# Kernel optimization log

Hardware: AMD Instinct MI355X
Metric: run time of the kernel (lower is better)

Reference implementation:

```python
import jax, jax.numpy as jnp
import numpy as np

B, S, D = 4, 1024, 1024
H, DK, DV = 16, 64, 64


def setup_inputs() -> dict:
    key = jax.random.key(0)
    ks = jax.random.split(key, 8)
    sc = 0.02
    return {
        "queries": jax.random.normal(ks[0], (B, S, D), jnp.float32),
        "keys": jax.random.normal(ks[1], (B, S, D), jnp.float32),
        "values": jax.random.normal(ks[2], (B, S, D), jnp.float32),
        "attn_bias": jax.random.normal(ks[3], (B, 1, S, S), jnp.float32),
        "Wq": jax.random.normal(ks[4], (H * DK, D), jnp.float32) * sc,
        "Wk": jax.random.normal(ks[5], (H * DK, D), jnp.float32) * sc,
        "Wv": jax.random.normal(ks[6], (H * DV, D), jnp.float32) * sc,
        "Wp": jax.random.normal(ks[7], (D, H * DV), jnp.float32) * sc,
    }


def reference(queries, keys, values, attn_bias, Wq, Wk, Wv, Wp):
    # Linear (no bias): x @ W.T, then split heads -> [B, H, S, d]
    q = (queries @ Wq.T).reshape(B, S, H, DK).transpose(0, 2, 1, 3)
    k = (keys @ Wk.T).reshape(B, S, H, DK).transpose(0, 2, 1, 3)
    v = (values @ Wv.T).reshape(B, S, H, DV).transpose(0, 2, 1, 3)
    # NOTE: original scales by d_model**-0.5, not d_key**-0.5
    scores = jnp.einsum("bhqd,bhkd->bhqk", q, k) * (D ** -0.5)
    scores = scores + attn_bias  # bias broadcasts over heads
    weights = jax.nn.softmax(scores, axis=-1)
    out = jnp.einsum("bhqk,bhkd->bhqd", weights, v)  # [B,H,S,DV]
    out = out.transpose(0, 2, 1, 3).reshape(B, S, H * DV)
    return out @ Wp.T
```

## Files before the change

### kernel.cpp

```cpp
#include <hip/hip_runtime.h>
#include <hip/hip_bf16.h>

typedef unsigned short u16;
typedef unsigned int u32;
typedef __attribute__((ext_vector_type(8))) short bf16x8;
typedef __attribute__((ext_vector_type(8))) u16 u16x8;
typedef __attribute__((ext_vector_type(4))) u16 u16x4;
typedef __attribute__((ext_vector_type(4))) u32 u32x4;
typedef __attribute__((ext_vector_type(4))) float f32x4;
typedef __attribute__((ext_vector_type(4))) _Float16 f16x4;
typedef __attribute__((ext_vector_type(8))) _Float16 f16x8;
typedef __attribute__((ext_vector_type(16))) float f32x16;

typedef const __attribute__((address_space(1))) void* gas1_t;
typedef __attribute__((address_space(3))) void* las3_t;

#define MFMA16(a,b,c) __builtin_amdgcn_mfma_f32_16x16x32_bf16((a),(b),(c),0,0,0)
#define MFMA32(a,b,c) __builtin_amdgcn_mfma_f32_32x32x16_bf16((a),(b),(c),0,0,0)

static constexpr int BB = 4, SS = 1024, DD = 1024, HH = 16;

static __device__ __forceinline__ u16 f2b(float x) {
  union { __hip_bfloat16 h; u16 u; } cv;
  cv.h = __float2bfloat16(x);
  return cv.u;
}
static __device__ __forceinline__ u32 pk2(float a, float b) {
  return (u32)f2b(a) | ((u32)f2b(b) << 16);
}

__global__ __launch_bounds__(256) void cvt_all(
    const float* __restrict__ q, const float* __restrict__ k, const float* __restrict__ v,
    const float* __restrict__ wq_, const float* __restrict__ wk_, const float* __restrict__ wv_,
    const float* __restrict__ wp_,
    u16* __restrict__ qb, u16* __restrict__ kb, u16* __restrict__ vb,
    u16* __restrict__ wqb, u16* __restrict__ wkb, u16* __restrict__ wvb, u16* __restrict__ wpb) {
  int bid = blockIdx.x;
  const float* s; u16* d; int off;
  if      (bid < 4096)  { s = q;   d = qb;  off = bid; }
  else if (bid < 8192)  { s = k;   d = kb;  off = bid - 4096; }
  else if (bid < 12288) { s = v;   d = vb;  off = bid - 8192; }
  else if (bid < 13312) { s = wq_; d = wqb; off = bid - 12288; }
  else if (bid < 14336) { s = wk_; d = wkb; off = bid - 13312; }
  else if (bid < 15360) { s = wv_; d = wvb; off = bid - 14336; }
  else                  { s = wp_; d = wpb; off = bid - 15360; }
  int i = (off * 256 + threadIdx.x) * 4;
  float4 val = *(const float4*)(s + i);
  u16x4 r = { f2b(val.x), f2b(val.y), f2b(val.z), f2b(val.w) };
  *(u16x4*)(d + i) = r;
}

__global__ __launch_bounds__(256) void cvt_bias(const float* __restrict__ src,
                                                _Float16* __restrict__ dst) {
  int i = (blockIdx.x * 256 + threadIdx.x) * 4;
  int row = i >> 10;
  int k = i & 1023;
  int kt = k >> 6, j = k & 63;
  int hi = (j >> 2) & 1, kb = j >> 5, rq = (j >> 3) & 3;
  int idx = hi * 32 + kb * 16 + rq * 4;
  int byte_in_slice = ((((idx >> 3) ^ (row & 7)) << 4) | ((idx & 7) << 1));
  float4 v = *(const float4*)(src + i);
  f16x4 r = { (_Float16)v.x, (_Float16)v.y, (_Float16)v.z, (_Float16)v.w };
  char* p = (char*)dst + ((size_t)row * 1024 + kt * 64) * 2 + byte_in_slice;
  *(f16x4*)p = r;
}

template<typename OT, bool VTRANS>
__global__ __launch_bounds__(256) void gemm_bt(
    const u16* __restrict__ Abase, const u16* __restrict__ Wbase, OT* __restrict__ Cbase,
    u16* __restrict__ Tout, int N, int K, size_t sA, size_t sW, size_t sC) {
  const u16* A = Abase + (size_t)blockIdx.z * sA;
  const u16* W = Wbase + (size_t)blockIdx.z * sW;
  OT* C = Cbase + (size_t)blockIdx.z * sC;

  __shared__ __align__(16) u16 As[128 * 64];
  __shared__ __align__(16) u16 Bs[128 * 64];

  const int tid = threadIdx.x;
  const int lane = tid & 63;
  const int wid = tid >> 6;
  const int g = lane >> 4;
  const int li = lane & 15;

  const int hw = blockIdx.x + (blockIdx.y << 3);
  const int L = ((hw & 7) << 5) + (hw >> 3);
  const int brow = (L >> 3) * 128;
  const int bcol = (L & 7) * 128;

  const int wr = (wid >> 1) * 64;
  const int wc = (wid & 1) * 64;

  const int srow = wid * 8 + (lane >> 3);
  const int schunk = (lane & 7) ^ (lane >> 3);
  const u16* ga0 = A + (size_t)(brow + srow) * K + schunk * 8;
  const u16* gw0 = W + (size_t)(bcol + srow) * K + schunk * 8;

  f32x4 acc[4][4] = {};

  for (int k0 = 0; k0 < K; k0 += 64) {
#pragma unroll
    for (int i = 0; i < 4; ++i) {
      __builtin_amdgcn_global_load_lds((gas1_t)(const void*)(ga0 + (size_t)(i * 32) * K + k0),
                                       (las3_t)(void*)(As + (i * 32 + wid * 8) * 64), 16, 0, 0);
      __builtin_amdgcn_global_load_lds((gas1_t)(const void*)(gw0 + (size_t)(i * 32) * K + k0),
                                       (las3_t)(void*)(Bs + (i * 32 + wid * 8) * 64), 16, 0, 0);
    }
    __syncthreads();

#pragma unroll
    for (int kk = 0; kk < 2; ++kk) {
      bf16x8 a[4], b[4];
#pragma unroll
      for (int m = 0; m < 4; ++m) {
        int row = wr + m * 16 + li;
        a[m] = *(const bf16x8*)&As[row * 64 + (((kk * 4 + g) ^ (li & 7)) << 3)];
      }
#pragma unroll
      for (int n = 0; n < 4; ++n) {
        int row = wc + n * 16 + li;
        b[n] = *(const bf16x8*)&Bs[row * 64 + (((kk * 4 + g) ^ (li & 7)) << 3)];
      }
#pragma unroll
      for (int m = 0; m < 4; ++m)
#pragma unroll
        for (int n = 0; n < 4; ++n)
          acc[m][n] = MFMA16(a[m], b[n], acc[m][n]);
    }
    __syncthreads();
  }

  if (VTRANS && blockIdx.z == 2) {
#pragma unroll
    for (int m = 0; m < 4; ++m) {
#pragma unroll
      for (int n = 0; n < 4; ++n) {
        int c = bcol + wc + n * 16 + li;
        int h_ = c >> 6, dv = c & 63;
        int r0 = brow + wr + m * 16 + g * 4;
        int b_ = r0 >> 10, s0 = r0 & 1023;
        u16x4 val = { f2b(acc[m][n][0]), f2b(acc[m][n][1]),
                      f2b(acc[m][n][2]), f2b(acc[m][n][3]) };
        *(u16x4*)&Tout[(size_t)((b_ * HH + h_) * 64 + dv) * SS + s0] = val;
      }
    }
  } else {
#pragma unroll
    for (int m = 0; m < 4; ++m)
#pragma unroll
      for (int n = 0; n < 4; ++n)
#pragma unroll
        for (int j = 0; j < 4; ++j) {
          int r = brow + wr + m * 16 + g * 4 + j;
          int c = bcol + wc + n * 16 + li;
          if constexpr (sizeof(OT) == 2) C[(size_t)r * N + c] = (OT)f2b(acc[m][n][j]);
          else                           C[(size_t)r * N + c] = acc[m][n][j];
        }
  }
}

__global__ __launch_bounds__(256) void attn_kernel(
    const u16* __restrict__ Q, const u16* __restrict__ K, const u16* __restrict__ Vt,
    const _Float16* __restrict__ bias16, u16* __restrict__ O) {
  __shared__ __align__(16) u16 kbuf[2][64 * 64];
  __shared__ __align__(16) u16 vbuf[2][64 * 64];
  __shared__ __align__(16) u16 bbuf[2][8192];

  const int tid = threadIdx.x;
  const int lane = tid & 63;
  const int wq = tid >> 6;
  const int hi = lane >> 5;
  const int ln = lane & 31;
  const u32 swz = (u32)(ln & 7) << 4;

  const int flat = blockIdx.x + (blockIdx.y << 3) + (blockIdx.z << 7);
  const int L = ((flat & 7) << 6) | (flat >> 3);
  const int qt = L & 7, h = (L >> 3) & 15, b = L >> 7;
  const int q0 = qt * 128;
  const int qrow = q0 + wq * 32 + ln;

  bf16x8 qf[4];
  {
    const u16* qp = Q + (size_t)(b * SS + qrow) * DD + h * 64 + hi * 8;
#pragma unroll
    for (int d = 0; d < 4; ++d) qf[d] = *(const bf16x8*)(qp + d * 16);
  }

  const int srow = (lane >> 3);
  const int spc = ((lane & 7) ^ srow) * 8;
  const u16* kgl = K + (size_t)(b * SS + wq * 16 + srow) * DD + h * 64 + spc;
  const u16* vgl = Vt + (size_t)((b * HH + h) * 64 + wq * 16 + srow) * SS + spc;

  const _Float16* bgl = bias16 + (size_t)(b * SS + q0 + wq * 32 + srow) * SS + (lane & 7) * 8;

  const int qq = wq * 32 + ln;
  int baddr[4];
#pragma unroll
  for (int g = 0; g < 4; ++g)
    baddr[g] = qq * 128 + (((hi * 4 + g) ^ (ln & 7)) << 4);

  {
    char* bd = (char*)bbuf[0] + wq * 4096;
#pragma unroll
    for (int i = 0; i < 4; ++i)
      __builtin_amdgcn_global_load_lds((gas1_t)(const void*)(bgl + (size_t)(i * 8) * SS),
                                       (las3_t)(void*)(bd + i * 1024), 16, 0, 0);
    char* kd = (char*)kbuf[0] + wq * 2048;
    char* vd = (char*)vbuf[0] + wq * 2048;
#pragma unroll
    for (int j = 0; j < 2; ++j) {
      __builtin_amdgcn_global_load_lds((gas1_t)(const void*)(kgl + (size_t)(j * 8) * DD),
                                       (las3_t)(void*)(kd + j * 1024), 16, 0, 0);
      __builtin_amdgcn_global_load_lds((gas1_t)(const void*)(vgl + (size_t)(j * 8) * SS),
                                       (las3_t)(void*)(vd + j * 1024), 16, 0, 0);
    }
  }
  __syncthreads();

  f32x16 o0 = {}, o1 = {};
  float m = -1e30f, lsum = 0.f;
  int cur = 0;

  for (int kt = 0; kt < 16; ++kt) {
    if (kt < 15) {
      char* bd = (char*)bbuf[cur ^ 1] + wq * 4096;
      const _Float16* bs = bgl + (kt + 1) * 64;
#pragma unroll
      for (int i = 0; i < 4; ++i)
        __builtin_amdgcn_global_load_lds((gas1_t)(const void*)(bs + (size_t)(i * 8) * SS),
                                         (las3_t)(void*)(bd + i * 1024), 16, 0, 0);
      char* kd = (char*)kbuf[cur ^ 1] + wq * 2048;
      char* vd = (char*)vbuf[cur ^ 1] + wq * 2048;
      const size_t k1 = (size_t)(kt + 1) * 64;
#pragma unroll
      for (int j = 0; j < 2; ++j) {
        __builtin_amdgcn_global_load_lds((gas1_t)(const void*)(kgl + (k1 + j * 8) * DD),
                                         (las3_t)(void*)(kd + j * 1024), 16, 0, 0);
        __builtin_amdgcn_global_load_lds((gas1_t)(const void*)(vgl + (size_t)(j * 8) * SS + k1),
                                         (las3_t)(void*)(vd + j * 1024), 16, 0, 0);
      }
    }

    const char* kb_base = (const char*)kbuf[cur];
    f32x16 s[2];
#pragma unroll
    for (int kb = 0; kb < 2; ++kb) {
      f32x16 acc = {};
#pragma unroll
      for (int d = 0; d < 4; ++d) {
        bf16x8 kf = *(const bf16x8*)(kb_base + (kb * 32 + ln) * 128 + (((u32)(d * 32 + hi * 16)) ^ swz));
        acc = MFMA32(kf, qf[d], acc);
      }
      s[kb] = acc;
    }

    {
      const char* bbr = (const char*)bbuf[cur];
#pragma unroll
      for (int g = 0; g < 4; ++g) {
        f16x8 bv = *(const f16x8*)(bbr + baddr[g]);
        const int kb = g >> 1, rq0 = (g & 1) * 2;
#pragma unroll
        for (int e = 0; e < 8; ++e)
          s[kb][(rq0 + (e >> 2)) * 4 + (e & 3)] =
              fmaf(s[kb][(rq0 + (e >> 2)) * 4 + (e & 3)], 0.03125f, (float)bv[e]);
      }
    }

    float mt = -1e30f;
#pragma unroll
    for (int r = 0; r < 16; ++r) { mt = fmaxf(mt, s[0][r]); mt = fmaxf(mt, s[1][r]); }
    mt = fmaxf(mt, __shfl_xor(mt, 32));

    bool resc = false;
    float fsc = 1.f;
    if (kt == 0) {
      m = mt;
    } else if (__any(mt > m + 8.f)) {
      float mn = fmaxf(m, mt);
      fsc = __expf(m - mn);
      m = mn;
      resc = true;
    }

    float rs = 0.f;
    u32 wv[2][8];
#pragma unroll
    for (int kb = 0; kb < 2; ++kb)
#pragma unroll
      for (int t = 0; t < 8; ++t) {
        float p0 = __expf(s[kb][2 * t] - m);
        float p1 = __expf(s[kb][2 * t + 1] - m);
        rs += p0 + p1;
        wv[kb][t] = pk2(p0, p1);
      }
    rs += __shfl_xor(rs, 32);
    lsum = lsum * fsc + rs;

    if (resc) {
#pragma unroll
      for (int j = 0; j < 16; ++j) {
        float fv = __shfl(fsc, (j & 3) + 8 * (j >> 2) + 4 * hi);
        o0[j] *= fv; o1[j] *= fv;
      }
    }

    const char* vb_base = (const char*)vbuf[cur];
#pragma unroll
    for (int ks = 0; ks < 4; ++ks) {
      const int kb = ks >> 1, i0 = (ks & 1) * 4;
      u32 sA = hi ? wv[kb][i0 + 0] : wv[kb][i0 + 2];
      u32 sB = hi ? wv[kb][i0 + 1] : wv[kb][i0 + 3];
      u32 rA = (u32)__shfl_xor((int)sA, 32);
      u32 rB = (u32)__shfl_xor((int)sB, 32);
      u32 e0 = hi ? rA : wv[kb][i0 + 0];
      u32 e1 = hi ? rB : wv[kb][i0 + 1];
      u32 e2 = hi ? wv[kb][i0 + 2] : rA;
      u32 e3 = hi ? wv[kb][i0 + 3] : rB;
      union { u32x4 u; bf16x8 v; } pc;
      pc.u = (u32x4){e0, e1, e2, e3};
      bf16x8 pa = pc.v;
#pragma unroll
      for (int nv = 0; nv < 2; ++nv) {
        bf16x8 vf = *(const bf16x8*)(vb_base + (nv * 32 + ln) * 128 + (((u32)(ks * 32 + hi * 16)) ^ swz));
        if (nv == 0) o0 = MFMA32(pa, vf, o0);
        else         o1 = MFMA32(pa, vf, o1);
      }
    }

    if (kt < 15) {
      __syncthreads();
      cur ^= 1;
    }
  }

  float inv = 1.0f / lsum;
#pragma unroll
  for (int j = 0; j < 16; ++j) {
    float iv = __shfl(inv, (j & 3) + 8 * (j >> 2) + 4 * hi);
    int q = q0 + wq * 32 + (j & 3) + 8 * (j >> 2) + 4 * hi;
    u16* op = O + (size_t)(b * SS + q) * DD + h * 64 + ln;
    op[0]  = f2b(o0[j] * iv);
    op[32] = f2b(o1[j] * iv);
  }
}

extern "C" void kernel_launch(void* const* d_in, const int* in_sizes, int n_in,
                              void* d_out, int out_size, void* d_ws, size_t ws_size,
                              hipStream_t stream) {
  const float* queries = (const float*)d_in[0];
  const float* keys    = (const float*)d_in[1];
  const float* values  = (const float*)d_in[2];
  const float* bias    = (const float*)d_in[3];
  const float* Wq      = (const float*)d_in[4];
  const float* Wk      = (const float*)d_in[5];
  const float* Wv      = (const float*)d_in[6];
  const float* Wp      = (const float*)d_in[7];
  float* out = (float*)d_out;

  char* ws = (char*)d_ws;
  const size_t MB = 1024 * 1024;
  u16* qb  = (u16*)(ws + 0 * MB);
  u16* kb  = (u16*)(ws + 8 * MB);
  u16* vb  = (u16*)(ws + 16 * MB);
  u16* wqb = (u16*)(ws + 24 * MB);
  u16* wkb = (u16*)(ws + 26 * MB);
  u16* wvb = (u16*)(ws + 28 * MB);
  u16* wpb = (u16*)(ws + 30 * MB);
  u16* Qb  = (u16*)(ws + 32 * MB);
  u16* Kb  = (u16*)(ws + 40 * MB);
  u16* Vtb = (u16*)(ws + 56 * MB);
  _Float16* bias16 = (_Float16*)(ws + 8 * MB);
  u16* Ob  = (u16*)(ws + 0 * MB);

  const int nAct = BB * SS * DD;
  const int nW = DD * DD;

  cvt_all<<<dim3(16384), dim3(256), 0, stream>>>(
      queries, keys, values, Wq, Wk, Wv, Wp,
      qb, kb, vb, wqb, wkb, wvb, wpb);

  gemm_bt<u16, true><<<dim3(8, 32, 3), dim3(256), 0, stream>>>(
      qb, wqb, Qb, Vtb, DD, DD, (size_t)nAct, (size_t)nW, (size_t)nAct);

  cvt_bias<<<dim3(4096), dim3(256), 0, stream>>>(bias, bias16);

  attn_kernel<<<dim3(8, 16, 4), dim3(256), 0, stream>>>(Qb, Kb, Vtb, bias16, Ob);

  gemm_bt<float, false><<<dim3(8, 32, 1), dim3(256), 0, stream>>>(
      Ob, wpb, out, nullptr, DD, DD, 0, 0, 0);
}
```

Measured before the change: 119.5 us.

## Fold bias conversion into cvt_all and load pre-tiled bias straight into registers

The bias fp32->fp16 conversion is merged into the cvt_all launch, removing one kernel launch. The converted bias is written in a per-thread fragment layout, so the attention kernel can load each thread's bias values from global memory straight into registers. This drops the LDS staging buffer and its reads. The next tile's bias is prefetched into registers, which adds register pressure but frees 32KB of LDS and may allow more blocks per CU. The bias buffer moves to its own workspace region at 48MB, so it no longer reuses the 8MB slot.

Result: slower. 122.0 us (+2.0%).

```diff
diff --git a/kernel.cpp b/kernel.cpp
--- a/kernel.cpp
+++ b/kernel.cpp
@@ -32,10 +32,28 @@
 __global__ __launch_bounds__(256) void cvt_all(
     const float* __restrict__ q, const float* __restrict__ k, const float* __restrict__ v,
     const float* __restrict__ wq_, const float* __restrict__ wk_, const float* __restrict__ wv_,
-    const float* __restrict__ wp_,
+    const float* __restrict__ wp_, const float* __restrict__ bias,
     u16* __restrict__ qb, u16* __restrict__ kb, u16* __restrict__ vb,
-    u16* __restrict__ wqb, u16* __restrict__ wkb, u16* __restrict__ wvb, u16* __restrict__ wpb) {
+    u16* __restrict__ wqb, u16* __restrict__ wkb, u16* __restrict__ wvb, u16* __restrict__ wpb,
+    _Float16* __restrict__ bias16) {
   int bid = blockIdx.x;
+  if (bid >= 16384) {
+    int i = ((bid - 16384) * 256 + threadIdx.x) * 4;
+    int row = i >> 10;
+    int kk_ = i & 1023;
+    int b_ = row >> 10, qq = row & 1023;
+    int qt = qq >> 7, wq = (qq >> 5) & 3, ln = qq & 31;
+    int kt = kk_ >> 6, kk = kk_ & 63;
+    int kbf = kk >> 5, rem = kk & 31, rq = rem >> 3, inner = rem & 7;
+    int hi = inner >> 2;
+    int g = kbf * 2 + (rq >> 1);
+    int ctid = wq * 64 + hi * 32 + ln;
+    size_t tile = ((size_t)(b_ * 8 + qt) * 16 + kt) << 13;
+    float4 val = *(const float4*)(bias + i);
+    f16x4 r = { (_Float16)val.x, (_Float16)val.y, (_Float16)val.z, (_Float16)val.w };
+    *(f16x4*)(bias16 + tile + g * 2048 + ctid * 8 + (rq & 1) * 4) = r;
+    return;
+  }
   const float* s; u16* d; int off;
   if      (bid < 4096)  { s = q;   d = qb;  off = bid; }
   else if (bid < 8192)  { s = k;   d = kb;  off = bid - 4096; }
@@ -50,21 +68,6 @@
   *(u16x4*)(d + i) = r;
 }
 
-__global__ __launch_bounds__(256) void cvt_bias(const float* __restrict__ src,
-                                                _Float16* __restrict__ dst) {
-  int i = (blockIdx.x * 256 + threadIdx.x) * 4;
-  int row = i >> 10;
-  int k = i & 1023;
-  int kt = k >> 6, j = k & 63;
-  int hi = (j >> 2) & 1, kb = j >> 5, rq = (j >> 3) & 3;
-  int idx = hi * 32 + kb * 16 + rq * 4;
-  int byte_in_slice = ((((idx >> 3) ^ (row & 7)) << 4) | ((idx & 7) << 1));
-  float4 v = *(const float4*)(src + i);
-  f16x4 r = { (_Float16)v.x, (_Float16)v.y, (_Float16)v.z, (_Float16)v.w };
-  char* p = (char*)dst + ((size_t)row * 1024 + kt * 64) * 2 + byte_in_slice;
-  *(f16x4*)p = r;
-}
-
 template<typename OT, bool VTRANS>
 __global__ __launch_bounds__(256) void gemm_bt(
     const u16* __restrict__ Abase, const u16* __restrict__ Wbase, OT* __restrict__ Cbase,
@@ -163,7 +166,6 @@
     const _Float16* __restrict__ bias16, u16* __restrict__ O) {
   __shared__ __align__(16) u16 kbuf[2][64 * 64];
   __shared__ __align__(16) u16 vbuf[2][64 * 64];
-  __shared__ __align__(16) u16 bbuf[2][8192];
 
   const int tid = threadIdx.x;
   const int lane = tid & 63;
@@ -190,20 +192,9 @@
   const u16* kgl = K + (size_t)(b * SS + wq * 16 + srow) * DD + h * 64 + spc;
   const u16* vgl = Vt + (size_t)((b * HH + h) * 64 + wq * 16 + srow) * SS + spc;
 
-  const _Float16* bgl = bias16 + (size_t)(b * SS + q0 + wq * 32 + srow) * SS + (lane & 7) * 8;
-
-  const int qq = wq * 32 + ln;
-  int baddr[4];
-#pragma unroll
-  for (int g = 0; g < 4; ++g)
-    baddr[g] = qq * 128 + (((hi * 4 + g) ^ (ln & 7)) << 4);
+  const _Float16* btile = bias16 + (((size_t)(b * 8 + qt) * 16) << 13) + tid * 8;
 
   {
-    char* bd = (char*)bbuf[0] + wq * 4096;
-#pragma unroll
-    for (int i = 0; i < 4; ++i)
-      __builtin_amdgcn_global_load_lds((gas1_t)(const void*)(bgl + (size_t)(i * 8) * SS),
-                                       (las3_t)(void*)(bd + i * 1024), 16, 0, 0);
     char* kd = (char*)kbuf[0] + wq * 2048;
     char* vd = (char*)vbuf[0] + wq * 2048;
 #pragma unroll
@@ -214,6 +205,10 @@
                                        (las3_t)(void*)(vd + j * 1024), 16, 0, 0);
     }
   }
+  f16x8 bbr[4], bbn[4];
+#pragma unroll
+  for (int g = 0; g < 4; ++g)
+    bbr[g] = *(const f16x8*)(btile + g * 2048);
   __syncthreads();
 
   f32x16 o0 = {}, o1 = {};
@@ -222,12 +217,6 @@
 
   for (int kt = 0; kt < 16; ++kt) {
     if (kt < 15) {
-      char* bd = (char*)bbuf[cur ^ 1] + wq * 4096;
-      const _Float16* bs = bgl + (kt + 1) * 64;
-#pragma unroll
-      for (int i = 0; i < 4; ++i)
-        __builtin_amdgcn_global_load_lds((gas1_t)(const void*)(bs + (size_t)(i * 8) * SS),
-                                         (las3_t)(void*)(bd + i * 1024), 16, 0, 0);
       char* kd = (char*)kbuf[cur ^ 1] + wq * 2048;
       char* vd = (char*)vbuf[cur ^ 1] + wq * 2048;
       const size_t k1 = (size_t)(kt + 1) * 64;
@@ -238,6 +227,10 @@
         __builtin_amdgcn_global_load_lds((gas1_t)(const void*)(vgl + (size_t)(j * 8) * SS + k1),
                                          (las3_t)(void*)(vd + j * 1024), 16, 0, 0);
       }
+      const _Float16* bt = btile + ((size_t)(kt + 1) << 13);
+#pragma unroll
+      for (int g = 0; g < 4; ++g)
+        bbn[g] = *(const f16x8*)(bt + g * 2048);
     }
 
     const char* kb_base = (const char*)kbuf[cur];
@@ -253,17 +246,13 @@
       s[kb] = acc;
     }
 
-    {
-      const char* bbr = (const char*)bbuf[cur];
-#pragma unroll
-      for (int g = 0; g < 4; ++g) {
-        f16x8 bv = *(const f16x8*)(bbr + baddr[g]);
-        const int kb = g >> 1, rq0 = (g & 1) * 2;
-#pragma unroll
-        for (int e = 0; e < 8; ++e)
-          s[kb][(rq0 + (e >> 2)) * 4 + (e & 3)] =
-              fmaf(s[kb][(rq0 + (e >> 2)) * 4 + (e & 3)], 0.03125f, (float)bv[e]);
-      }
+#pragma unroll
+    for (int g = 0; g < 4; ++g) {
+      const int kb = g >> 1, rq0 = (g & 1) * 2;
+#pragma unroll
+      for (int e = 0; e < 8; ++e)
+        s[kb][(rq0 + (e >> 2)) * 4 + (e & 3)] =
+            fmaf(s[kb][(rq0 + (e >> 2)) * 4 + (e & 3)], 0.03125f, (float)bbr[g][e]);
     }
 
     float mt = -1e30f;
@@ -330,6 +319,8 @@
     if (kt < 15) {
       __syncthreads();
       cur ^= 1;
+#pragma unroll
+      for (int g = 0; g < 4; ++g) bbr[g] = bbn[g];
     }
   }
 
@@ -368,22 +359,20 @@
   u16* wpb = (u16*)(ws + 30 * MB);
   u16* Qb  = (u16*)(ws + 32 * MB);
   u16* Kb  = (u16*)(ws + 40 * MB);
+  _Float16* bias16 = (_Float16*)(ws + 48 * MB);
   u16* Vtb = (u16*)(ws + 56 * MB);
-  _Float16* bias16 = (_Float16*)(ws + 8 * MB);
   u16* Ob  = (u16*)(ws + 0 * MB);
 
   const int nAct = BB * SS * DD;
   const int nW = DD * DD;
 
-  cvt_all<<<dim3(16384), dim3(256), 0, stream>>>(
-      queries, keys, values, Wq, Wk, Wv, Wp,
-      qb, kb, vb, wqb, wkb, wvb, wpb);
+  cvt_all<<<dim3(20480), dim3(256), 0, stream>>>(
+      queries, keys, values, Wq, Wk, Wv, Wp, bias,
+      qb, kb, vb, wqb, wkb, wvb, wpb, bias16);
 
   gemm_bt<u16, true><<<dim3(8, 32, 3), dim3(256), 0, stream>>>(
       qb, wqb, Qb, Vtb, DD, DD, (size_t)nAct, (size_t)nW, (size_t)nAct);
 
-  cvt_bias<<<dim3(4096), dim3(256), 0, stream>>>(bias, bias16);
-
   attn_kernel<<<dim3(8, 16, 4), dim3(256), 0, stream>>>(Qb, Kb, Vtb, bias16, Ob);
 
   gemm_bt<float, false><<<dim3(8, 32, 1), dim3(256), 0, stream>>>(
```
